# Optimization experiments

Measured on AMD Instinct MI355X. Metric: run time of the kernel, lower is better.

## Reference

```python
import jax, jax.numpy as jnp
import numpy as np

DIM_IN = 25
H = 128        # num_neurons
P = 8000       # num_pixel
BS = 32
NEG_SLOPE = 0.01  # torch LeakyReLU default


def _leaky(x):
    return jnp.where(x >= 0, x, NEG_SLOPE * x)


def setup_inputs() -> dict:
    key = jax.random.key(0)
    ks = jax.random.split(key, 7)
    x = jax.random.normal(ks[0], (BS, DIM_IN), dtype=jnp.float32)
    # Stacked per-pixel MLP params (kaiming-ish scale to keep values sane)
    W1 = jax.random.normal(ks[1], (P, DIM_IN, H), dtype=jnp.float32) / np.sqrt(DIM_IN)
    b1 = jax.random.normal(ks[2], (P, H), dtype=jnp.float32) * 0.01
    W2 = jax.random.normal(ks[3], (P, H, H), dtype=jnp.float32) / np.sqrt(H)
    b2 = jax.random.normal(ks[4], (P, H), dtype=jnp.float32) * 0.01
    W3 = jax.random.normal(ks[5], (P, H), dtype=jnp.float32) / np.sqrt(H)
    b3 = jax.random.normal(ks[6], (P,), dtype=jnp.float32) * 0.01
    return {"x": x, "W1": W1, "b1": b1, "W2": W2, "b2": b2, "W3": W3, "b3": b3}


def reference(x, W1, b1, W2, b2, W3, b3):
    # h1: [bs, P, H] -- every pixel MLP sees the same x
    h1 = _leaky(jnp.einsum('bd,pdh->bph', x, W1) + b1[None])
    h2 = _leaky(jnp.einsum('bph,phk->bpk', h1, W2) + b2[None])
    # final Linear(num_neurons, 1) -> scalar per pixel -> y[bs, P]
    y = jnp.einsum('bph,ph->bp', h2, W3) + b3[None]
    return y
```

## Files before the change

### kernel.cpp

```cpp
#include <hip/hip_runtime.h>


constexpr int DIM_IN = 25;
constexpr int H      = 128;
constexpr int P      = 8000;
constexpr int BS     = 32;
constexpr float NEG  = 0.01f;

typedef short  short4v __attribute__((ext_vector_type(4)));
typedef short  short8v __attribute__((ext_vector_type(8)));
typedef float  f32x4   __attribute__((ext_vector_type(4)));

__device__ __forceinline__ float leaky(float v) { return v >= 0.f ? v : NEG * v; }

__device__ __forceinline__ short bf_rne(float f) {
    unsigned u = __builtin_bit_cast(unsigned, f);
    return (short)((u + 0x7fffu + ((u >> 16) & 1u)) >> 16);
}
__device__ __forceinline__ short bf_rna(float f) {
    unsigned u = __builtin_bit_cast(unsigned, f);
    return (short)((u + 0x8000u) >> 16);
}

#define STAGE_TILE(BUF, KT) {                                                  \
    const float* gsrc_ = W2p + (size_t)(KT) * (32 * H) + (t << 2);             \
    float* dst_ = &w2t[BUF][0];                                                \
    _Pragma("unroll")                                                          \
    for (int q_ = 0; q_ < 16; ++q_)                                            \
        __builtin_amdgcn_global_load_lds(                                      \
            (const __attribute__((address_space(1))) unsigned*)(gsrc_ + q_ * 256), \
            (__attribute__((address_space(3))) unsigned*)(dst_ + q_ * 256),    \
            16, 0, 0); }

#define CONSUME_TILE(BUF, KB) {                                                \
    const short8v a0_ = *reinterpret_cast<const short8v*>(                     \
        &h1b[cc][32 * (KB) + 8 * gg]);                                         \
    const short8v a1_ = *reinterpret_cast<const short8v*>(                     \
        &h1b[16 + cc][32 * (KB) + 8 * gg]);                                    \
    const float* tb_ = &w2t[BUF][8 * gg * H + cc];                             \
    _Pragma("unroll")                                                          \
    for (int nb_ = 0; nb_ < 8; ++nb_) {                                        \
        const float* col_ = tb_ + 16 * nb_;                                    \
        short8v bf_;                                                           \
        bf_[0] = bf_rna(col_[0 * H]); bf_[1] = bf_rna(col_[1 * H]);            \
        bf_[2] = bf_rna(col_[2 * H]); bf_[3] = bf_rna(col_[3 * H]);            \
        bf_[4] = bf_rna(col_[4 * H]); bf_[5] = bf_rna(col_[5 * H]);            \
        bf_[6] = bf_rna(col_[6 * H]); bf_[7] = bf_rna(col_[7 * H]);            \
        ac0[nb_] = __builtin_amdgcn_mfma_f32_16x16x32_bf16(a0_, bf_, ac0[nb_], 0, 0, 0); \
        ac1[nb_] = __builtin_amdgcn_mfma_f32_16x16x32_bf16(a1_, bf_, ac1[nb_], 0, 0, 0); \
    } }

__global__ __launch_bounds__(64, 1) void pixel_mlp_kernel(
    const float* __restrict__ x,
    const float* __restrict__ W1,
    const float* __restrict__ b1,
    const float* __restrict__ W2,
    const float* __restrict__ b2,
    const float* __restrict__ W3,
    const float* __restrict__ b3,
    float* __restrict__ y)
{
    const int p  = blockIdx.x;
    const int t  = threadIdx.x;
    const int cc = t & 15;
    const int gg = t >> 4;
    const int c0 = cc << 2;
    const int r0 = gg << 3;

    __shared__ float sxT[DIM_IN][BS];
    __shared__ short h1b[BS][H];
    __shared__ float w2t[2][32 * H];

    const float* W1p = W1 + (size_t)p * (DIM_IN * H);
    const float* W2p = W2 + (size_t)p * (H * H);

    const float4 b1l = *reinterpret_cast<const float4*>(b1 + (size_t)p * H + c0);
    const float4 b1h = *reinterpret_cast<const float4*>(b1 + (size_t)p * H + 64 + c0);
    float b2v[8], w3v[8];
    #pragma unroll
    for (int nb = 0; nb < 8; ++nb) {
        b2v[nb] = b2[(size_t)p * H + 16 * nb + cc];
        w3v[nb] = W3[(size_t)p * H + 16 * nb + cc];
    }
    const float b3s = b3[p];
    asm volatile("" ::: "memory");

    STAGE_TILE(0, 0)
    STAGE_TILE(1, 1)
    asm volatile("" ::: "memory");

    for (int i = t; i < DIM_IN * BS; i += 64)
        sxT[i >> 5][i & 31] = x[(i & 31) * DIM_IN + (i >> 5)];
    asm volatile("s_waitcnt lgkmcnt(0)" ::: "memory");

    float aL1[8][8];
    {
        const float bv[8] = {b1l.x, b1l.y, b1l.z, b1l.w, b1h.x, b1h.y, b1h.z, b1h.w};
        #pragma unroll
        for (int i = 0; i < 8; ++i)
            #pragma unroll
            for (int c = 0; c < 8; ++c)
                aL1[i][c] = bv[c];
    }
    #pragma unroll 5
    for (int d = 0; d < DIM_IN; ++d) {
        const float4 a0 = *reinterpret_cast<const float4*>(&sxT[d][r0]);
        const float4 a1 = *reinterpret_cast<const float4*>(&sxT[d][r0 + 4]);
        const float av[8] = {a0.x, a0.y, a0.z, a0.w, a1.x, a1.y, a1.z, a1.w};
        const float4 wl = *reinterpret_cast<const float4*>(W1p + d * H + c0);
        const float4 wh = *reinterpret_cast<const float4*>(W1p + d * H + 64 + c0);
        const float wv[8] = {wl.x, wl.y, wl.z, wl.w, wh.x, wh.y, wh.z, wh.w};
        #pragma unroll
        for (int i = 0; i < 8; ++i)
            #pragma unroll
            for (int c = 0; c < 8; ++c)
                aL1[i][c] += av[i] * wv[c];
    }

    #pragma unroll
    for (int i = 0; i < 8; ++i) {
        short4v lo, hi;
        lo[0] = bf_rne(leaky(aL1[i][0])); lo[1] = bf_rne(leaky(aL1[i][1]));
        lo[2] = bf_rne(leaky(aL1[i][2])); lo[3] = bf_rne(leaky(aL1[i][3]));
        hi[0] = bf_rne(leaky(aL1[i][4])); hi[1] = bf_rne(leaky(aL1[i][5]));
        hi[2] = bf_rne(leaky(aL1[i][6])); hi[3] = bf_rne(leaky(aL1[i][7]));
        *reinterpret_cast<short4v*>(&h1b[r0 + i][4 * cc])      = lo;
        *reinterpret_cast<short4v*>(&h1b[r0 + i][64 + 4 * cc]) = hi;
    }
    asm volatile("s_waitcnt lgkmcnt(0)" ::: "memory");
    __builtin_amdgcn_sched_barrier(0);

    f32x4 ac0[8], ac1[8];
    #pragma unroll
    for (int nb = 0; nb < 8; ++nb) {
        ac0[nb] = (f32x4){0.f, 0.f, 0.f, 0.f};
        ac1[nb] = (f32x4){0.f, 0.f, 0.f, 0.f};
    }

    asm volatile("s_waitcnt vmcnt(16)" ::: "memory");
    CONSUME_TILE(0, 0)
    asm volatile("s_waitcnt lgkmcnt(0)" ::: "memory");
    STAGE_TILE(0, 2)
    asm volatile("s_waitcnt vmcnt(16)" ::: "memory");
    CONSUME_TILE(1, 1)
    asm volatile("s_waitcnt lgkmcnt(0)" ::: "memory");
    STAGE_TILE(1, 3)
    asm volatile("s_waitcnt vmcnt(16)" ::: "memory");
    CONSUME_TILE(0, 2)
    asm volatile("s_waitcnt vmcnt(0)" ::: "memory");
    CONSUME_TILE(1, 3)

    float s0[4], s1[4];
    #pragma unroll
    for (int q = 0; q < 4; ++q) {
        float a = 0.f, b = 0.f;
        #pragma unroll
        for (int nb = 0; nb < 8; ++nb) {
            a += leaky(ac0[nb][q] + b2v[nb]) * w3v[nb];
            b += leaky(ac1[nb][q] + b2v[nb]) * w3v[nb];
        }
        s0[q] = a; s1[q] = b;
    }
    #pragma unroll
    for (int m = 8; m >= 1; m >>= 1) {
        #pragma unroll
        for (int q = 0; q < 4; ++q) {
            s0[q] += __shfl_xor(s0[q], m);
            s1[q] += __shfl_xor(s1[q], m);
        }
    }
    if (cc == 0) {
        #pragma unroll
        for (int q = 0; q < 4; ++q) {
            y[(size_t)(4 * gg + q) * P + p]      = s0[q] + b3s;
            y[(size_t)(16 + 4 * gg + q) * P + p] = s1[q] + b3s;
        }
    }
}

extern "C" void kernel_launch(void* const* d_in, const int* in_sizes, int n_in,
                              void* d_out, int out_size, void* d_ws, size_t ws_size,
                              hipStream_t stream) {
    const float* x  = (const float*)d_in[0];
    const float* W1 = (const float*)d_in[1];
    const float* b1 = (const float*)d_in[2];
    const float* W2 = (const float*)d_in[3];
    const float* b2 = (const float*)d_in[4];
    const float* W3 = (const float*)d_in[5];
    const float* b3 = (const float*)d_in[6];
    float* y = (float*)d_out;

    pixel_mlp_kernel<<<dim3(P), dim3(64), 0, stream>>>(x, W1, b1, W2, b2, W3, b3, y);
}
```

Before: 161.9 us.

## Halve W2 LDS staging tiles to 32x64 to allow more resident blocks

Each W2 K-tile is split into two half-width column tiles of 32x64, which halves the double-buffered LDS staging area. Launch bounds now target two blocks per SM so more single-wave blocks can be resident to hide the streaming latency of W2. The unrolled 4-stage schedule becomes a rolled loop over 8 half-tile consume/stage steps with smaller vmcnt waits. The cost is more, finer-grained synchronisation points and a tighter register budget from the launch bound.

```diff
diff --git a/kernel.cpp b/kernel.cpp
--- a/kernel.cpp
+++ b/kernel.cpp
@@ -22,35 +22,38 @@
     return (short)((u + 0x8000u) >> 16);
 }
 
-#define STAGE_TILE(BUF, KT) {                                                  \
-    const float* gsrc_ = W2p + (size_t)(KT) * (32 * H) + (t << 2);             \
+#define STAGE_TILE(BUF, KT, HF) {                                              \
+    const float* gsrc_ = W2p + (size_t)(KT) * (32 * H) + (HF) * 64             \
+                         + (t >> 4) * H + ((t & 15) << 2);                     \
     float* dst_ = &w2t[BUF][0];                                                \
     _Pragma("unroll")                                                          \
-    for (int q_ = 0; q_ < 16; ++q_)                                            \
+    for (int q_ = 0; q_ < 8; ++q_)                                             \
         __builtin_amdgcn_global_load_lds(                                      \
-            (const __attribute__((address_space(1))) unsigned*)(gsrc_ + q_ * 256), \
+            (const __attribute__((address_space(1))) unsigned*)(gsrc_ + q_ * 4 * H), \
             (__attribute__((address_space(3))) unsigned*)(dst_ + q_ * 256),    \
             16, 0, 0); }
 
-#define CONSUME_TILE(BUF, KB) {                                                \
+#define CONSUME_TILE(BUF, KT, HF) {                                            \
     const short8v a0_ = *reinterpret_cast<const short8v*>(                     \
-        &h1b[cc][32 * (KB) + 8 * gg]);                                         \
+        &h1b[cc][32 * (KT) + 8 * gg]);                                         \
     const short8v a1_ = *reinterpret_cast<const short8v*>(                     \
-        &h1b[16 + cc][32 * (KB) + 8 * gg]);                                    \
-    const float* tb_ = &w2t[BUF][8 * gg * H + cc];                             \
+        &h1b[16 + cc][32 * (KT) + 8 * gg]);                                    \
+    const float* tb_ = &w2t[BUF][8 * gg * 64 + cc];                            \
     _Pragma("unroll")                                                          \
-    for (int nb_ = 0; nb_ < 8; ++nb_) {                                        \
+    for (int nb_ = 0; nb_ < 4; ++nb_) {                                        \
         const float* col_ = tb_ + 16 * nb_;                                    \
         short8v bf_;                                                           \
-        bf_[0] = bf_rna(col_[0 * H]); bf_[1] = bf_rna(col_[1 * H]);            \
-        bf_[2] = bf_rna(col_[2 * H]); bf_[3] = bf_rna(col_[3 * H]);            \
-        bf_[4] = bf_rna(col_[4 * H]); bf_[5] = bf_rna(col_[5 * H]);            \
-        bf_[6] = bf_rna(col_[6 * H]); bf_[7] = bf_rna(col_[7 * H]);            \
-        ac0[nb_] = __builtin_amdgcn_mfma_f32_16x16x32_bf16(a0_, bf_, ac0[nb_], 0, 0, 0); \
-        ac1[nb_] = __builtin_amdgcn_mfma_f32_16x16x32_bf16(a1_, bf_, ac1[nb_], 0, 0, 0); \
+        bf_[0] = bf_rna(col_[0 * 64]); bf_[1] = bf_rna(col_[1 * 64]);          \
+        bf_[2] = bf_rna(col_[2 * 64]); bf_[3] = bf_rna(col_[3 * 64]);          \
+        bf_[4] = bf_rna(col_[4 * 64]); bf_[5] = bf_rna(col_[5 * 64]);          \
+        bf_[6] = bf_rna(col_[6 * 64]); bf_[7] = bf_rna(col_[7 * 64]);          \
+        ac0[4 * (HF) + nb_] = __builtin_amdgcn_mfma_f32_16x16x32_bf16(         \
+            a0_, bf_, ac0[4 * (HF) + nb_], 0, 0, 0);                           \
+        ac1[4 * (HF) + nb_] = __builtin_amdgcn_mfma_f32_16x16x32_bf16(         \
+            a1_, bf_, ac1[4 * (HF) + nb_], 0, 0, 0);                           \
     } }
 
-__global__ __launch_bounds__(64, 1) void pixel_mlp_kernel(
+__global__ __launch_bounds__(64, 2) void pixel_mlp_kernel(
     const float* __restrict__ x,
     const float* __restrict__ W1,
     const float* __restrict__ b1,
@@ -69,7 +72,7 @@
 
     __shared__ float sxT[DIM_IN][BS];
     __shared__ short h1b[BS][H];
-    __shared__ float w2t[2][32 * H];
+    __shared__ float w2t[2][32 * 64];
 
     const float* W1p = W1 + (size_t)p * (DIM_IN * H);
     const float* W2p = W2 + (size_t)p * (H * H);
@@ -85,8 +88,8 @@
     const float b3s = b3[p];
     asm volatile("" ::: "memory");
 
-    STAGE_TILE(0, 0)
-    STAGE_TILE(1, 1)
+    STAGE_TILE(0, 0, 0)
+    STAGE_TILE(1, 0, 1)
     asm volatile("" ::: "memory");
 
     for (int i = t; i < DIM_IN * BS; i += 64)
@@ -137,18 +140,21 @@
         ac1[nb] = (f32x4){0.f, 0.f, 0.f, 0.f};
     }
 
-    asm volatile("s_waitcnt vmcnt(16)" ::: "memory");
-    CONSUME_TILE(0, 0)
-    asm volatile("s_waitcnt lgkmcnt(0)" ::: "memory");
-    STAGE_TILE(0, 2)
-    asm volatile("s_waitcnt vmcnt(16)" ::: "memory");
-    CONSUME_TILE(1, 1)
-    asm volatile("s_waitcnt lgkmcnt(0)" ::: "memory");
-    STAGE_TILE(1, 3)
-    asm volatile("s_waitcnt vmcnt(16)" ::: "memory");
-    CONSUME_TILE(0, 2)
+    #pragma unroll 1
+    for (int kt = 0; kt < 3; ++kt) {
+        asm volatile("s_waitcnt vmcnt(8)" ::: "memory");
+        CONSUME_TILE(0, kt, 0)
+        asm volatile("s_waitcnt lgkmcnt(0)" ::: "memory");
+        STAGE_TILE(0, kt + 1, 0)
+        asm volatile("s_waitcnt vmcnt(8)" ::: "memory");
+        CONSUME_TILE(1, kt, 1)
+        asm volatile("s_waitcnt lgkmcnt(0)" ::: "memory");
+        STAGE_TILE(1, kt + 1, 1)
+    }
+    asm volatile("s_waitcnt vmcnt(8)" ::: "memory");
+    CONSUME_TILE(0, 3, 0)
     asm volatile("s_waitcnt vmcnt(0)" ::: "memory");
-    CONSUME_TILE(1, 3)
+    CONSUME_TILE(1, 3, 1)
 
     float s0[4], s1[4];
     #pragma unroll
```

New measurement: 137.3 us. -15.2%, faster.

## Switch W2 GEMM to 32x32x16 MFMA with small swizzled LDS tiles

Applied to the files above, without the earlier changes.

Restructures the second-layer matmul around 32x32x16 bf16 MFMA with four 16-wide accumulators. W2 is staged in 16x64 half-tiles (8KB double buffer instead of 32KB) over a rolled loop, h1 is stored in LDS with an XOR swizzle, and launch bounds now allow two blocks per CU. The goal is to cut LDS usage and improve occupancy and bank-conflict behaviour so memory streaming overlaps better. The cost is many smaller stages with more waitcnt synchronization points and a longer shuffle reduction over 16 values per lane.

```diff
diff --git a/kernel.cpp b/kernel.cpp
--- a/kernel.cpp
+++ b/kernel.cpp
@@ -9,7 +9,7 @@
 
 typedef short  short4v __attribute__((ext_vector_type(4)));
 typedef short  short8v __attribute__((ext_vector_type(8)));
-typedef float  f32x4   __attribute__((ext_vector_type(4)));
+typedef float  f32x16  __attribute__((ext_vector_type(16)));
 
 __device__ __forceinline__ float leaky(float v) { return v >= 0.f ? v : NEG * v; }
 
@@ -22,35 +22,35 @@
     return (short)((u + 0x8000u) >> 16);
 }
 
-#define STAGE_TILE(BUF, KT) {                                                  \
-    const float* gsrc_ = W2p + (size_t)(KT) * (32 * H) + (t << 2);             \
+#define STAGE_T(BUF, KT, HF) {                                                 \
+    const float* gsrc_ = W2p + (size_t)(16 * (KT) + (t >> 4)) * H              \
+                         + 64 * (HF) + ((t & 15) << 2);                        \
     float* dst_ = &w2t[BUF][0];                                                \
     _Pragma("unroll")                                                          \
-    for (int q_ = 0; q_ < 16; ++q_)                                            \
+    for (int i_ = 0; i_ < 4; ++i_)                                             \
         __builtin_amdgcn_global_load_lds(                                      \
-            (const __attribute__((address_space(1))) unsigned*)(gsrc_ + q_ * 256), \
-            (__attribute__((address_space(3))) unsigned*)(dst_ + q_ * 256),    \
+            (const __attribute__((address_space(1))) unsigned*)(gsrc_ + (size_t)i_ * 4 * H), \
+            (__attribute__((address_space(3))) unsigned*)(dst_ + i_ * 256),    \
             16, 0, 0); }
 
-#define CONSUME_TILE(BUF, KB) {                                                \
-    const short8v a0_ = *reinterpret_cast<const short8v*>(                     \
-        &h1b[cc][32 * (KB) + 8 * gg]);                                         \
-    const short8v a1_ = *reinterpret_cast<const short8v*>(                     \
-        &h1b[16 + cc][32 * (KB) + 8 * gg]);                                    \
-    const float* tb_ = &w2t[BUF][8 * gg * H + cc];                             \
+#define CONSUME_T(BUF, KT, HF) {                                               \
+    const int ao_ = lo * 256 + 32 * (KT) + 16 * hi;                            \
+    const short8v a_ = *reinterpret_cast<const short8v*>(                      \
+        (const char*)h1b + (ao_ ^ ((lo & 7) << 4)));                           \
+    const float* tb_ = &w2t[BUF][hi * 512 + lo];                               \
     _Pragma("unroll")                                                          \
-    for (int nb_ = 0; nb_ < 8; ++nb_) {                                        \
-        const float* col_ = tb_ + 16 * nb_;                                    \
+    for (int n2_ = 0; n2_ < 2; ++n2_) {                                        \
+        const float* col_ = tb_ + 32 * n2_;                                    \
         short8v bf_;                                                           \
-        bf_[0] = bf_rna(col_[0 * H]); bf_[1] = bf_rna(col_[1 * H]);            \
-        bf_[2] = bf_rna(col_[2 * H]); bf_[3] = bf_rna(col_[3 * H]);            \
-        bf_[4] = bf_rna(col_[4 * H]); bf_[5] = bf_rna(col_[5 * H]);            \
-        bf_[6] = bf_rna(col_[6 * H]); bf_[7] = bf_rna(col_[7 * H]);            \
-        ac0[nb_] = __builtin_amdgcn_mfma_f32_16x16x32_bf16(a0_, bf_, ac0[nb_], 0, 0, 0); \
-        ac1[nb_] = __builtin_amdgcn_mfma_f32_16x16x32_bf16(a1_, bf_, ac1[nb_], 0, 0, 0); \
+        bf_[0] = bf_rna(col_[0]);   bf_[1] = bf_rna(col_[64]);                 \
+        bf_[2] = bf_rna(col_[128]); bf_[3] = bf_rna(col_[192]);                \
+        bf_[4] = bf_rna(col_[256]); bf_[5] = bf_rna(col_[320]);                \
+        bf_[6] = bf_rna(col_[384]); bf_[7] = bf_rna(col_[448]);                \
+        acc[2 * (HF) + n2_] = __builtin_amdgcn_mfma_f32_32x32x16_bf16(         \
+            a_, bf_, acc[2 * (HF) + n2_], 0, 0, 0);                            \
     } }
 
-__global__ __launch_bounds__(64, 1) void pixel_mlp_kernel(
+__global__ __launch_bounds__(64, 2) void pixel_mlp_kernel(
     const float* __restrict__ x,
     const float* __restrict__ W1,
     const float* __restrict__ b1,
@@ -66,27 +66,29 @@
     const int gg = t >> 4;
     const int c0 = cc << 2;
     const int r0 = gg << 3;
+    const int lo = t & 31;
+    const int hi = t >> 5;
 
     __shared__ float sxT[DIM_IN][BS];
     __shared__ short h1b[BS][H];
-    __shared__ float w2t[2][32 * H];
+    __shared__ float w2t[2][16 * 64];
 
     const float* W1p = W1 + (size_t)p * (DIM_IN * H);
     const float* W2p = W2 + (size_t)p * (H * H);
 
     const float4 b1l = *reinterpret_cast<const float4*>(b1 + (size_t)p * H + c0);
     const float4 b1h = *reinterpret_cast<const float4*>(b1 + (size_t)p * H + 64 + c0);
-    float b2v[8], w3v[8];
+    float b2v[4], w3v[4];
     #pragma unroll
-    for (int nb = 0; nb < 8; ++nb) {
-        b2v[nb] = b2[(size_t)p * H + 16 * nb + cc];
-        w3v[nb] = W3[(size_t)p * H + 16 * nb + cc];
+    for (int nb = 0; nb < 4; ++nb) {
+        b2v[nb] = b2[(size_t)p * H + 32 * nb + lo];
+        w3v[nb] = W3[(size_t)p * H + 32 * nb + lo];
     }
     const float b3s = b3[p];
     asm volatile("" ::: "memory");
 
-    STAGE_TILE(0, 0)
-    STAGE_TILE(1, 1)
+    STAGE_T(0, 0, 0)
+    STAGE_T(1, 0, 1)
     asm volatile("" ::: "memory");
 
     for (int i = t; i < DIM_IN * BS; i += 64)
@@ -119,61 +121,60 @@
 
     #pragma unroll
     for (int i = 0; i < 8; ++i) {
-        short4v lo, hi;
-        lo[0] = bf_rne(leaky(aL1[i][0])); lo[1] = bf_rne(leaky(aL1[i][1]));
-        lo[2] = bf_rne(leaky(aL1[i][2])); lo[3] = bf_rne(leaky(aL1[i][3]));
-        hi[0] = bf_rne(leaky(aL1[i][4])); hi[1] = bf_rne(leaky(aL1[i][5]));
-        hi[2] = bf_rne(leaky(aL1[i][6])); hi[3] = bf_rne(leaky(aL1[i][7]));
-        *reinterpret_cast<short4v*>(&h1b[r0 + i][4 * cc])      = lo;
-        *reinterpret_cast<short4v*>(&h1b[r0 + i][64 + 4 * cc]) = hi;
+        short4v lov, hiv;
+        lov[0] = bf_rne(leaky(aL1[i][0])); lov[1] = bf_rne(leaky(aL1[i][1]));
+        lov[2] = bf_rne(leaky(aL1[i][2])); lov[3] = bf_rne(leaky(aL1[i][3]));
+        hiv[0] = bf_rne(leaky(aL1[i][4])); hiv[1] = bf_rne(leaky(aL1[i][5]));
+        hiv[2] = bf_rne(leaky(aL1[i][6])); hiv[3] = bf_rne(leaky(aL1[i][7]));
+        const int ro = (r0 + i) * 256;
+        const int sz = ((r0 + i) & 7) << 4;
+        *reinterpret_cast<short4v*>((char*)h1b + ((ro + 8 * cc) ^ sz))       = lov;
+        *reinterpret_cast<short4v*>((char*)h1b + ((ro + 128 + 8 * cc) ^ sz)) = hiv;
     }
     asm volatile("s_waitcnt lgkmcnt(0)" ::: "memory");
     __builtin_amdgcn_sched_barrier(0);
 
-    f32x4 ac0[8], ac1[8];
+    f32x16 acc[4];
     #pragma unroll
-    for (int nb = 0; nb < 8; ++nb) {
-        ac0[nb] = (f32x4){0.f, 0.f, 0.f, 0.f};
-        ac1[nb] = (f32x4){0.f, 0.f, 0.f, 0.f};
+    for (int nb = 0; nb < 4; ++nb)
+        acc[nb] = (f32x16)(0.f);
+
+    #pragma unroll 1
+    for (int kt = 0; kt < 7; ++kt) {
+        asm volatile("s_waitcnt vmcnt(4)" ::: "memory");
+        CONSUME_T(0, kt, 0)
+        asm volatile("s_waitcnt lgkmcnt(0)" ::: "memory");
+        STAGE_T(0, kt + 1, 0)
+        asm volatile("s_waitcnt vmcnt(4)" ::: "memory");
+        CONSUME_T(1, kt, 1)
+        asm volatile("s_waitcnt lgkmcnt(0)" ::: "memory");
+        STAGE_T(1, kt + 1, 1)
     }
+    asm volatile("s_waitcnt vmcnt(4)" ::: "memory");
+    CONSUME_T(0, 7, 0)
+    asm volatile("s_waitcnt vmcnt(0)" ::: "memory");
+    CONSUME_T(1, 7, 1)
 
-    asm volatile("s_waitcnt vmcnt(16)" ::: "memory");
-    CONSUME_TILE(0, 0)
-    asm volatile("s_waitcnt lgkmcnt(0)" ::: "memory");
-    STAGE_TILE(0, 2)
-    asm volatile("s_waitcnt vmcnt(16)" ::: "memory");
-    CONSUME_TILE(1, 1)
-    asm volatile("s_waitcnt lgkmcnt(0)" ::: "memory");
-    STAGE_TILE(1, 3)
-    asm volatile("s_waitcnt vmcnt(16)" ::: "memory");
-    CONSUME_TILE(0, 2)
-    asm volatile("s_waitcnt vmcnt(0)" ::: "memory");
-    CONSUME_TILE(1, 3)
-
-    float s0[4], s1[4];
+    float s[16];
     #pragma unroll
-    for (int q = 0; q < 4; ++q) {
-        float a = 0.f, b = 0.f;
+    for (int reg = 0; reg < 16; ++reg) {
+        float acc_s = 0.f;
         #pragma unroll
-        for (int nb = 0; nb < 8; ++nb) {
-            a += leaky(ac0[nb][q] + b2v[nb]) * w3v[nb];
-            b += leaky(ac1[nb][q] + b2v[nb]) * w3v[nb];
-        }
-        s0[q] = a; s1[q] = b;
+        for (int nb = 0; nb < 4; ++nb)
+            acc_s += leaky(acc[nb][reg] + b2v[nb]) * w3v[nb];
+        s[reg] = acc_s;
     }
     #pragma unroll
-    for (int m = 8; m >= 1; m >>= 1) {
+    for (int m = 16; m >= 1; m >>= 1) {
         #pragma unroll
-        for (int q = 0; q < 4; ++q) {
-            s0[q] += __shfl_xor(s0[q], m);
-            s1[q] += __shfl_xor(s1[q], m);
-        }
+        for (int reg = 0; reg < 16; ++reg)
+            s[reg] += __shfl_xor(s[reg], m);
     }
-    if (cc == 0) {
+    if (lo == 0) {
         #pragma unroll
-        for (int q = 0; q < 4; ++q) {
-            y[(size_t)(4 * gg + q) * P + p]      = s0[q] + b3s;
-            y[(size_t)(16 + 4 * gg + q) * P + p] = s1[q] + b3s;
+        for (int reg = 0; reg < 16; ++reg) {
+            const int r = (reg & 3) + 8 * (reg >> 2) + 4 * hi;
+            y[(size_t)r * P + p] = s[reg] + b3s;
         }
     }
 }
```

Measured after the change: 130.9 us. 1.24x faster.
